# Kernel optimization log

Measured on AMD Instinct MI355X. Metric: run time of the kernel, lower is better.

## Reference

```python
import jax, jax.numpy as jnp
import numpy as np

B = 64        # batch
L = 256       # latent_dim
H = 1024      # hidden
D = 1024      # mask dim
BAND = 16     # half-bandwidth of sparsity mask
M = 2 * BAND + 1  # max nnz per row (=33)


def _banded_mask_idx():
    """Build a banded (D,D) 0/1 mask and per-row column indices (D,M), -1 padded."""
    r = np.arange(D)
    mask = (np.abs(r[:, None] - r[None, :]) <= BAND).astype(np.float32)
    idx = np.full((D, M), -1, dtype=np.int32)
    for i in range(D):
        cols = np.nonzero(mask[i])[0]
        idx[i, :len(cols)] = cols
    return mask, idx


def setup_inputs() -> dict:
    key = jax.random.key(0)
    kz, k1, kb1, k2, kb2 = jax.random.split(key, 5)
    mask_np, idx_np = _banded_mask_idx()
    return {
        "z": jax.random.normal(kz, (B, L), dtype=jnp.float32),
        "mask": jnp.asarray(mask_np),
        "W1": jax.random.normal(k1, (L, H), dtype=jnp.float32) * 0.05,
        "b1": jax.random.normal(kb1, (H,), dtype=jnp.float32) * 0.05,
        "W2": jax.random.normal(k2, (H, D * M), dtype=jnp.float32) * 0.02,
        "b2": jax.random.normal(kb2, (D * M,), dtype=jnp.float32) * 0.02,
        "idx": jnp.asarray(idx_np),
    }


def reference(z, mask, W1, b1, W2, b2, idx):
    b = z.shape[0]
    # 2-layer MLP with exact (erf) GELU, as in nn.GELU()
    h = jax.nn.gelu(z @ W1 + b1, approximate=False)
    v = (h @ W2 + b2).reshape(b, D, M)          # (B, D, M)
    # scatter predicted values onto the mask support (unique targets -> add == set)
    valid = idx >= 0                             # (D, M)
    jc = jnp.where(valid, idx, 0)                # clamp -1 padding to col 0
    rows = jnp.broadcast_to(jnp.arange(D)[:, None], (D, M))
    vals = jnp.where(valid, v, jnp.zeros((), v.dtype))
    k = jnp.zeros((b, D, D), dtype=z.dtype).at[:, rows, jc].add(vals)
    # symmetrize, add identity, re-apply mask
    k = 0.5 * (k + jnp.swapaxes(k, -1, -2))
    k = k + jnp.eye(D, dtype=z.dtype)
    return k * mask[None, :, :]
```

## Files before the change

kernel.cpp:

```cpp
#include <hip/hip_runtime.h>
#include <math.h>

#define BATCH 64
#define LDIM  256
#define HDIM  1024
#define DDIM  1024
#define BAND  16
#define MNZ   33
#define NN    (DDIM*MNZ)

typedef float v4f __attribute__((ext_vector_type(4)));

__global__ __launch_bounds__(256) void k1_h(const float* __restrict__ z,
                                            const float* __restrict__ W1,
                                            const float* __restrict__ b1,
                                            float* __restrict__ ht) {
    __shared__ float zs[LDIM];
    const int t = threadIdx.x;
    const int b = blockIdx.y;
    const int j = blockIdx.x * 256 + t;
    zs[t] = z[b * LDIM + t];
    __syncthreads();
    float acc = b1[j];
#pragma unroll 8
    for (int l = 0; l < LDIM; ++l)
        acc = fmaf(zs[l], W1[l * HDIM + j], acc);
    float g = 0.5f * acc * (1.0f + erff(acc * 0.70710678118654752f));
    ht[(size_t)j * BATCH + b] = g;
}

__global__ __launch_bounds__(256) void k2_v(const float* __restrict__ W2,
                                            const float* __restrict__ b2,
                                            const float* __restrict__ ht,
                                            float* __restrict__ v) {
    const int lane = threadIdx.x & 63;
    const int col  = blockIdx.x * 64 + lane;
    const int bg = __builtin_amdgcn_readfirstlane((int)(threadIdx.x >> 6));
    const int b0 = bg * 16;

    float acc[16];
#pragma unroll
    for (int j = 0; j < 16; ++j) acc[j] = 0.0f;

    const float* __restrict__ wp = W2 + col;
    const float* __restrict__ hp = ht + b0;

    for (int kk = 0; kk < HDIM; ++kk) {
        const float w = wp[(size_t)kk * NN];
        const float4* __restrict__ h4 = (const float4*)(hp + kk * BATCH);
        const float4 a = h4[0], b = h4[1], c = h4[2], d = h4[3];
        acc[0]  = fmaf(a.x, w, acc[0]);
        acc[1]  = fmaf(a.y, w, acc[1]);
        acc[2]  = fmaf(a.z, w, acc[2]);
        acc[3]  = fmaf(a.w, w, acc[3]);
        acc[4]  = fmaf(b.x, w, acc[4]);
        acc[5]  = fmaf(b.y, w, acc[5]);
        acc[6]  = fmaf(b.z, w, acc[6]);
        acc[7]  = fmaf(b.w, w, acc[7]);
        acc[8]  = fmaf(c.x, w, acc[8]);
        acc[9]  = fmaf(c.y, w, acc[9]);
        acc[10] = fmaf(c.z, w, acc[10]);
        acc[11] = fmaf(c.w, w, acc[11]);
        acc[12] = fmaf(d.x, w, acc[12]);
        acc[13] = fmaf(d.y, w, acc[13]);
        acc[14] = fmaf(d.z, w, acc[14]);
        acc[15] = fmaf(d.w, w, acc[15]);
    }

    const float bias = b2[col];
#pragma unroll
    for (int j = 0; j < 16; ++j)
        v[(size_t)(b0 + j) * NN + col] = acc[j] + bias;
}

__global__ __launch_bounds__(256) void k3_out(const float* __restrict__ v,
                                              float* __restrict__ out) {
    const int tid = threadIdx.x;
#pragma unroll
    for (int r = 0; r < 4; ++r) {
        const int rowid = blockIdx.x * 4 + r;
        const int b = rowid >> 10;
        const int i = rowid & (DDIM - 1);
        const int j0 = tid * 4;
        v4f res = (v4f){0.f, 0.f, 0.f, 0.f};
        if (j0 + 3 >= i - BAND && j0 <= i + BAND) {
            const int lo_i = (i > BAND) ? (i - BAND) : 0;
            const float* __restrict__ vb = v + (size_t)b * NN;
#pragma unroll
            for (int c = 0; c < 4; ++c) {
                const int j = j0 + c;
                const int d = j - i;
                float x = 0.0f;
                if (d >= -BAND && d <= BAND) {
                    const int lo_j = (j > BAND) ? (j - BAND) : 0;
                    x = 0.5f * (vb[i * MNZ + (j - lo_i)] + vb[j * MNZ + (i - lo_j)]);
                    if (d == 0) x += 1.0f;
                }
                res[c] = x;
            }
        }
        v4f* dst = ((v4f*)out) + (size_t)rowid * (DDIM / 4) + tid;
        __builtin_nontemporal_store(res, dst);
    }
}

extern "C" void kernel_launch(void* const* d_in, const int* in_sizes, int n_in,
                              void* d_out, int out_size, void* d_ws, size_t ws_size,
                              hipStream_t stream) {
    const float* z  = (const float*)d_in[0];
    const float* W1 = (const float*)d_in[2];
    const float* b1 = (const float*)d_in[3];
    const float* W2 = (const float*)d_in[4];
    const float* b2 = (const float*)d_in[5];

    float* ht = (float*)d_ws;
    float* v  = ht + BATCH * HDIM;
    float* out = (float*)d_out;

    k1_h  <<<dim3(4, 64), 256, 0, stream>>>(z, W1, b1, ht);
    k2_v  <<<dim3(NN / 64), 256, 0, stream>>>(W2, b2, ht, v);
    k3_out<<<dim3((BATCH * DDIM) / 4), 256, 0, stream>>>(v, out);
}
```

Baseline: 513.0 us.

## Split-K the W2 GEMM with 4-column vector tiles and reduce partials in scatter

The second-layer GEMM kernel now gives each lane four adjacent output columns, loaded as one vector, and splits the K dimension across a second grid axis (up to 4 slices, chosen to fit the workspace). Each slice writes its partial sums to its own buffer, and the output kernel adds the slices while it gathers the band values. The aim is more register reuse of the broadcast h values per W2 load, and more parallelism when the column-tiled grid shrinks by four. The cost is extra partial-buffer writes and reads: up to four copies of the B×D×M array.

```diff
diff --git a/kernel.cpp b/kernel.cpp
--- a/kernel.cpp
+++ b/kernel.cpp
@@ -32,49 +32,47 @@
 __global__ __launch_bounds__(256) void k2_v(const float* __restrict__ W2,
                                             const float* __restrict__ b2,
                                             const float* __restrict__ ht,
-                                            float* __restrict__ v) {
+                                            float* __restrict__ vpart,
+                                            int kchunk) {
     const int lane = threadIdx.x & 63;
-    const int col  = blockIdx.x * 64 + lane;
-    const int bg = __builtin_amdgcn_readfirstlane((int)(threadIdx.x >> 6));
-    const int b0 = bg * 16;
+    const int wave = __builtin_amdgcn_readfirstlane((int)(threadIdx.x >> 6));
+    const int c0 = blockIdx.x * 256 + lane * 4;
+    const int b0 = wave * 16;
+    const int ks = blockIdx.y * kchunk;
 
-    float acc[16];
+    v4f acc[16];
 #pragma unroll
-    for (int j = 0; j < 16; ++j) acc[j] = 0.0f;
+    for (int j = 0; j < 16; ++j) acc[j] = (v4f){0.f, 0.f, 0.f, 0.f};
 
-    const float* __restrict__ wp = W2 + col;
-    const float* __restrict__ hp = ht + b0;
+    const float* __restrict__ wp = W2 + (size_t)ks * NN + c0;
+    const float* __restrict__ hp = ht + (size_t)ks * BATCH + b0;
 
-    for (int kk = 0; kk < HDIM; ++kk) {
-        const float w = wp[(size_t)kk * NN];
-        const float4* __restrict__ h4 = (const float4*)(hp + kk * BATCH);
-        const float4 a = h4[0], b = h4[1], c = h4[2], d = h4[3];
-        acc[0]  = fmaf(a.x, w, acc[0]);
-        acc[1]  = fmaf(a.y, w, acc[1]);
-        acc[2]  = fmaf(a.z, w, acc[2]);
-        acc[3]  = fmaf(a.w, w, acc[3]);
-        acc[4]  = fmaf(b.x, w, acc[4]);
-        acc[5]  = fmaf(b.y, w, acc[5]);
-        acc[6]  = fmaf(b.z, w, acc[6]);
-        acc[7]  = fmaf(b.w, w, acc[7]);
-        acc[8]  = fmaf(c.x, w, acc[8]);
-        acc[9]  = fmaf(c.y, w, acc[9]);
-        acc[10] = fmaf(c.z, w, acc[10]);
-        acc[11] = fmaf(c.w, w, acc[11]);
-        acc[12] = fmaf(d.x, w, acc[12]);
-        acc[13] = fmaf(d.y, w, acc[13]);
-        acc[14] = fmaf(d.z, w, acc[14]);
-        acc[15] = fmaf(d.w, w, acc[15]);
+#pragma unroll 2
+    for (int kk = 0; kk < kchunk; ++kk) {
+        const v4f w4 = *(const v4f*)(wp + (size_t)kk * NN);
+        const float* __restrict__ hh = hp + (size_t)kk * BATCH;
+#pragma unroll
+        for (int j = 0; j < 16; ++j)
+            acc[j] += hh[j] * w4;
     }
 
-    const float bias = b2[col];
+    float* __restrict__ vo = vpart + (size_t)blockIdx.y * (BATCH * (size_t)NN)
+                             + (size_t)b0 * NN + c0;
+    if (blockIdx.y == 0) {
+        const v4f bias = *(const v4f*)(b2 + c0);
 #pragma unroll
-    for (int j = 0; j < 16; ++j)
-        v[(size_t)(b0 + j) * NN + col] = acc[j] + bias;
+        for (int j = 0; j < 16; ++j)
+            *(v4f*)(vo + (size_t)j * NN) = acc[j] + bias;
+    } else {
+#pragma unroll
+        for (int j = 0; j < 16; ++j)
+            *(v4f*)(vo + (size_t)j * NN) = acc[j];
+    }
 }
 
-__global__ __launch_bounds__(256) void k3_out(const float* __restrict__ v,
-                                              float* __restrict__ out) {
+__global__ __launch_bounds__(256) void k3_out(const float* __restrict__ vpart,
+                                              float* __restrict__ out,
+                                              int nsplit) {
     const int tid = threadIdx.x;
 #pragma unroll
     for (int r = 0; r < 4; ++r) {
@@ -85,7 +83,7 @@
         v4f res = (v4f){0.f, 0.f, 0.f, 0.f};
         if (j0 + 3 >= i - BAND && j0 <= i + BAND) {
             const int lo_i = (i > BAND) ? (i - BAND) : 0;
-            const float* __restrict__ vb = v + (size_t)b * NN;
+            const float* __restrict__ vb = vpart + (size_t)b * NN;
 #pragma unroll
             for (int c = 0; c < 4; ++c) {
                 const int j = j0 + c;
@@ -93,7 +91,12 @@
                 float x = 0.0f;
                 if (d >= -BAND && d <= BAND) {
                     const int lo_j = (j > BAND) ? (j - BAND) : 0;
-                    x = 0.5f * (vb[i * MNZ + (j - lo_i)] + vb[j * MNZ + (i - lo_j)]);
+                    float s = 0.0f;
+                    for (int sN = 0; sN < nsplit; ++sN) {
+                        const float* __restrict__ vs = vb + (size_t)sN * (BATCH * (size_t)NN);
+                        s += vs[i * MNZ + (j - lo_i)] + vs[j * MNZ + (i - lo_j)];
+                    }
+                    x = 0.5f * s;
                     if (d == 0) x += 1.0f;
                 }
                 res[c] = x;
@@ -114,10 +117,16 @@
     const float* b2 = (const float*)d_in[5];
 
     float* ht = (float*)d_ws;
-    float* v  = ht + BATCH * HDIM;
+    float* vpart = ht + BATCH * HDIM;
     float* out = (float*)d_out;
 
+    const size_t base = (size_t)BATCH * HDIM * sizeof(float);
+    const size_t per_slice = (size_t)BATCH * NN * sizeof(float);
+    int nsplit = 4;
+    while (nsplit > 1 && base + (size_t)nsplit * per_slice > ws_size) nsplit >>= 1;
+    const int kchunk = HDIM / nsplit;
+
     k1_h  <<<dim3(4, 64), 256, 0, stream>>>(z, W1, b1, ht);
-    k2_v  <<<dim3(NN / 64), 256, 0, stream>>>(W2, b2, ht, v);
-    k3_out<<<dim3((BATCH * DDIM) / 4), 256, 0, stream>>>(v, out);
+    k2_v  <<<dim3(NN / 256, nsplit), 256, 0, stream>>>(W2, b2, ht, vpart, kchunk);
+    k3_out<<<dim3((BATCH * DDIM) / 4), 256, 0, stream>>>(vpart, out, nsplit);
 }
```

Result: slower. 570.8 us (+11.3%).
